# Kernel optimization log

Hardware: AMD Instinct MI355X
Metric: run time of the kernel (lower is better)

The kernel has to match this reference:

```python
import jax, jax.numpy as jnp
import numpy as np

KEY_SIZE = 256
EPS = 1e-8  # torch F.cosine_similarity default eps


def setup_inputs() -> dict:
    key = jax.random.key(0)
    k1, k2 = jax.random.split(key)
    B, M, K, V = 2048, 100000, KEY_SIZE, 256
    query = jax.random.normal(k1, (B, K), dtype=jnp.float32)
    memory = jax.random.normal(k2, (M, K + V), dtype=jnp.float32)
    return {"query": query, "memory": memory}


def reference(query, memory):
    # memory: [M, K+V] -> keys [M, K], values [M, V]
    keys = memory[:, :KEY_SIZE]
    values = memory[:, KEY_SIZE:]
    # cosine similarity: (q . k) / max(|q|*|k|, eps)  -> [B, M]
    dots = jnp.einsum('bk,mk->bm', query, keys)
    qn = jnp.linalg.norm(query, axis=1)  # [B]
    kn = jnp.linalg.norm(keys, axis=1)   # [M]
    sims = dots / jnp.maximum(qn[:, None] * kn[None, :], EPS)
    # top-1 over memory dim, then gather values -> [B, V]
    idx = jnp.argmax(sims, axis=1)
    return values[idx]
```

## Files before the change

kernel.cpp:

```cpp
#include <hip/hip_runtime.h>
#include <hip/hip_fp16.h>
#include <float.h>

#define MKEY 256
#define NMEM 100000
#define NPAD 100096
#define NQ   2048
#define BM 128
#define BN 128
#define NTILES 782
#define BLKPAD 800
#define MTILES 16
#define GRID (128 * 98)
#define KEYBLOCKS (NPAD / 4)
#define QS (127.0f / 6.0f)
#define SS2 ((6.0f / 127.0f) * (6.0f / 127.0f))

typedef int i32x4 __attribute__((ext_vector_type(4)));

__device__ inline void gll16(const void* g, void* l) {
  __builtin_amdgcn_global_load_lds(
      (const __attribute__((address_space(1))) unsigned*)g,
      (__attribute__((address_space(3))) unsigned*)l, 16, 0, 0);
}

__device__ inline int pack_i8x4(float4 v) {
  int c0 = max(-127, min(127, __float2int_rn(v.x * QS)));
  int c1 = max(-127, min(127, __float2int_rn(v.y * QS)));
  int c2 = max(-127, min(127, __float2int_rn(v.z * QS)));
  int c3 = max(-127, min(127, __float2int_rn(v.w * QS)));
  return (c0 & 255) | ((c1 & 255) << 8) | ((c2 & 255) << 16) | ((c3 & 255) << 24);
}

__device__ inline int dot4i8(int a, int b) {
  int s = 0;
#pragma unroll
  for (int k = 0; k < 4; ++k) {
    const int av = (a << (24 - 8 * k)) >> 24;
    const int bv = (b << (24 - 8 * k)) >> 24;
    s += av * bv;
  }
  return s;
}

__global__ void convert(const float* __restrict__ q, const float* __restrict__ mem,
                        int* __restrict__ qi, int* __restrict__ ki,
                        float* __restrict__ rkn) {
  const int b = blockIdx.x;
  if (b >= KEYBLOCKS) {
    const int i = (b - KEYBLOCKS) * 256 + threadIdx.x;
    const float4 v = *(const float4*)&q[(size_t)i * 4];
    qi[i] = pack_i8x4(v);
    return;
  }
  const int t = threadIdx.x, lane = t & 63, w = t >> 6;
  const int row = b * 4 + w;
  if (row < NMEM) {
    const float4 v = *(const float4*)&mem[(long)row * 512 + lane * 4];
    const float ss0 = v.x * v.x + v.y * v.y + v.z * v.z + v.w * v.w;
    ki[(size_t)row * 64 + lane] = pack_i8x4(v);
    float ss = ss0;
#pragma unroll
    for (int off = 32; off >= 1; off >>= 1) ss += __shfl_xor(ss, off, 64);
    if (lane == 0) rkn[row] = 1.0f / sqrtf(fmaxf(ss, 1e-30f));
  } else {
    ki[(size_t)row * 64 + lane] = 0;
    if (lane == 0) rkn[row] = 0.f;
  }
}

__global__ __launch_bounds__(256, 4) void gemm_screen(
    const int* __restrict__ qi, const int* __restrict__ ki,
    const float* __restrict__ rkn, float* __restrict__ bmaxB) {
  __shared__ __align__(128) char Ab[BM * 128];
  __shared__ __align__(128) char Bb[BN * 128];
  __shared__ float cand[BM][2];

  const int id = blockIdx.x;
  const int mtile = (id >> 3) & 15;
  const int ntile = (id & 7) + 8 * (id >> 7);
  if (ntile >= NTILES) return;

  const int t = threadIdx.x;
  const int w = t >> 6;
  const int lane = t & 63;
  const int wr = w >> 1, wc = w & 1;
  const int q16 = lane >> 4, l16 = lane & 15;
  const int l8 = lane >> 3, c8 = lane & 7;

  const int swz = (c8 ^ l8) * 16;
  int soff[8];
#pragma unroll
  for (int c = 0; c < 8; ++c)
    soff[c] = ((w & 1) * 64 + c * 8 + l8) * 256 + swz;
  const char* asrc = (const char*)((w < 2) ? qi : ki) +
                     (size_t)(((w < 2) ? mtile : ntile) * 128) * 256;
  char* adst = ((w < 2) ? Ab : Bb) + (w & 1) * 8192;

  i32x4 acc[4][4];
#pragma unroll
  for (int i = 0; i < 4; i++)
#pragma unroll
    for (int j = 0; j < 4; j++) acc[i][j] = (i32x4){0, 0, 0, 0};

  int pc[2];
#pragma unroll
  for (int ks = 0; ks < 2; ++ks) pc[ks] = (((ks * 4 + q16) ^ (l16 & 7))) * 16;

#pragma unroll
  for (int s = 0; s < 2; ++s) {
    __syncthreads();
#pragma unroll
    for (int c = 0; c < 8; ++c)
      gll16(asrc + s * 128 + soff[c], adst + c * 1024);
    __syncthreads();
#pragma unroll
    for (int ks = 0; ks < 2; ++ks) {
      i32x4 av[4], bv[4];
#pragma unroll
      for (int i = 0; i < 4; i++)
        av[i] = *(const i32x4*)&Ab[(64 * wr + 16 * i + l16) * 128 + pc[ks]];
#pragma unroll
      for (int j = 0; j < 4; j++)
        bv[j] = *(const i32x4*)&Bb[(64 * wc + 16 * j + l16) * 128 + pc[ks]];
#pragma unroll
      for (int i = 0; i < 4; i++)
#pragma unroll
        for (int j = 0; j < 4; j++)
          acc[i][j] = __builtin_amdgcn_mfma_i32_16x16x64_i8(av[i], bv[j], acc[i][j], 0, 0, 0);
    }
  }

  int ncol[4];
  float rk[4];
#pragma unroll
  for (int j = 0; j < 4; j++) {
    ncol[j] = ntile * BN + 64 * wc + 16 * j + l16;
    rk[j] = (ncol[j] < NMEM) ? rkn[ncol[j]] * SS2 : 0.f;
  }
#pragma unroll
  for (int i = 0; i < 4; i++) {
#pragma unroll
    for (int r = 0; r < 4; r++) {
      float m = -FLT_MAX;
#pragma unroll
      for (int j = 0; j < 4; j++)
        if (ncol[j] < NMEM) m = fmaxf(m, (float)acc[i][j][r] * rk[j]);
#pragma unroll
      for (int off = 1; off < 16; off <<= 1)
        m = fmaxf(m, __shfl_xor(m, off, 64));
      if (l16 == 0) cand[64 * wr + 16 * i + 4 * q16 + r][wc] = m;
    }
  }
  __syncthreads();
  if (t < BM) {
    float v = fmaxf(cand[t][0], cand[t][1]);
    bmaxB[(size_t)ntile * NQ + mtile * BM + t] = v;
  }
}

__global__ __launch_bounds__(256) void transpose_blk(const float* __restrict__ in,
                                                     float* __restrict__ outp) {
  __shared__ float tl[32][33];
  const int bid = blockIdx.x;
  const int ntt = bid % 25, qt = bid / 25;
  const int r0 = ntt * 32, c0 = qt * 32;
  const int tx = threadIdx.x & 31, ty = threadIdx.x >> 5;
#pragma unroll
  for (int k = 0; k < 4; ++k) {
    const int r = r0 + ty + 8 * k;
    tl[ty + 8 * k][tx] = (r < NTILES) ? in[(size_t)r * NQ + c0 + tx] : -FLT_MAX;
  }
  __syncthreads();
#pragma unroll
  for (int k = 0; k < 4; ++k) {
    const int qq = c0 + ty + 8 * k;
    const int nt = r0 + tx;
    if (nt < NTILES) outp[(size_t)qq * BLKPAD + nt] = tl[tx][ty + 8 * k];
  }
}

__global__ __launch_bounds__(256) void rescore_gather(
    const float* __restrict__ q, const float* __restrict__ mem,
    const int* __restrict__ qi8, const int* __restrict__ ki8,
    const float* __restrict__ rkn, const float* __restrict__ bmaxQ,
    float* __restrict__ out) {
  __shared__ float red2[4];
  __shared__ int blist[64];
  __shared__ int nblk;
  __shared__ int rlist[256];
  __shared__ int nrow;
  __shared__ double wb[4];
  __shared__ int wbi[4];
  __shared__ int widx;

  const int qid = blockIdx.x;
  const int t = threadIdx.x, w = t >> 6, lane = t & 63;

  const float4 qv = *(const float4*)&q[(size_t)qid * 256 + lane * 4];
  float ss = qv.x * qv.x + qv.y * qv.y + qv.z * qv.z + qv.w * qv.w;
#pragma unroll
  for (int off = 32; off >= 1; off >>= 1) ss += __shfl_xor(ss, off, 64);
  const float qn = sqrtf(ss);
  const float margin = 1.8e-2f * qn;

  int4 qreg[4];
#pragma unroll
  for (int k = 0; k < 4; ++k)
    qreg[k] = *(const int4*)&qi8[(size_t)qid * 64 + (lane & 3) * 16 + k * 4];

  if (t == 0) { nblk = 0; nrow = 0; }
  const float* bq = &bmaxQ[(size_t)qid * BLKPAD];

  float gm = -FLT_MAX;
  for (int i = t; i < NTILES; i += 256) gm = fmaxf(gm, bq[i]);
#pragma unroll
  for (int off = 32; off >= 1; off >>= 1) gm = fmaxf(gm, __shfl_xor(gm, off, 64));
  if (lane == 0) red2[w] = gm;
  __syncthreads();
  gm = fmaxf(fmaxf(red2[0], red2[1]), fmaxf(red2[2], red2[3]));
  const float thresh = gm - margin;

  for (int i = t; i < NTILES; i += 256)
    if (bq[i] >= thresh) {
      int p = atomicAdd(&nblk, 1);
      if (p < 64) blist[p] = i;
    }
  __syncthreads();
  const int nb_ = min(nblk, 64);

  for (int c = 0; c < nb_; ++c) {
    const int nt = blist[c];
#pragma unroll
    for (int pass = 0; pass < 2; ++pass) {
      const int row = nt * 128 + pass * 64 + w * 16 + (lane >> 2);
      int idot = 0;
      if (row < NMEM) {
#pragma unroll
        for (int k = 0; k < 4; ++k) {
          const int4 kv = *(const int4*)&ki8[(size_t)row * 64 + (lane & 3) * 16 + k * 4];
          idot += dot4i8(kv.x, qreg[k].x) + dot4i8(kv.y, qreg[k].y) +
                  dot4i8(kv.z, qreg[k].z) + dot4i8(kv.w, qreg[k].w);
        }
      }
      idot += __shfl_xor(idot, 1, 64);
      idot += __shfl_xor(idot, 2, 64);
      if ((lane & 3) == 0 && row < NMEM) {
        const float sh = (float)idot * (rkn[row] * SS2);
        if (sh >= thresh) {
          int p = atomicAdd(&nrow, 1);
          if (p < 256) rlist[p] = row;
        }
      }
    }
  }
  __syncthreads();
  const int nr = min(nrow, 256);

  double bestv = -1e300;
  int bestidx = 0x7fffffff;
  for (int c = w; c < nr; c += 4) {
    const int row = rlist[c];
    const float4 kv = *(const float4*)&mem[(size_t)row * 512 + lane * 4];
    double d = (double)kv.x * qv.x + (double)kv.y * qv.y +
               (double)kv.z * qv.z + (double)kv.w * qv.w;
    double s2 = (double)kv.x * kv.x + (double)kv.y * kv.y +
                (double)kv.z * kv.z + (double)kv.w * kv.w;
#pragma unroll
    for (int off = 32; off >= 1; off >>= 1) {
      d += __shfl_xor(d, off, 64);
      s2 += __shfl_xor(s2, off, 64);
    }
    if (lane == 0) {
      const double score = d / sqrt(s2 > 1e-300 ? s2 : 1e-300);
      if (score > bestv || (score == bestv && row < bestidx)) {
        bestv = score;
        bestidx = row;
      }
    }
  }
  if (lane == 0) { wb[w] = bestv; wbi[w] = bestidx; }
  __syncthreads();
  if (t == 0) {
    double bv = wb[0];
    int bi = wbi[0];
#pragma unroll
    for (int w2 = 1; w2 < 4; ++w2)
      if (wb[w2] > bv || (wb[w2] == bv && wbi[w2] < bi)) {
        bv = wb[w2];
        bi = wbi[w2];
      }
    widx = bi;
  }
  __syncthreads();
  out[(size_t)qid * 256 + t] = mem[(size_t)widx * 512 + 256 + t];
}

extern "C" void kernel_launch(void* const* d_in, const int* in_sizes, int n_in,
                              void* d_out, int out_size, void* d_ws, size_t ws_size,
                              hipStream_t stream) {
  const float* query = (const float*)d_in[0];
  const float* memory = (const float*)d_in[1];
  float* out = (float*)d_out;

  char* p = (char*)d_ws;
  int* qi = (int*)p; p += (size_t)NQ * 64 * 4;
  int* ki = (int*)p; p += (size_t)NPAD * 64 * 4;
  float* rkn = (float*)p; p += (size_t)NPAD * 4;
  float* bmaxB = (float*)p; p += (size_t)NTILES * NQ * 4;
  float* bmaxQ = (float*)p; p += (size_t)NQ * BLKPAD * 4;

  hipLaunchKernelGGL(convert, dim3(KEYBLOCKS + NQ * MKEY / 1024), dim3(256), 0, stream,
                     query, memory, qi, ki, rkn);
  hipLaunchKernelGGL(gemm_screen, dim3(GRID), dim3(256), 0, stream, qi, ki, rkn, bmaxB);
  hipLaunchKernelGGL(transpose_blk, dim3(25 * 64), dim3(256), 0, stream, bmaxB, bmaxQ);
  hipLaunchKernelGGL(rescore_gather, dim3(NQ), dim3(256), 0, stream,
                     query, memory, qi, ki, rkn, bmaxQ, out);
}
```

Measured before the change: 431.2 us.

## Add 16-row group maxima to screen rescoring and use sdot4 for int8 dots

The GEMM screen now also writes a per-(query, 16-key group) maximum of the int8 scores. It stages the accumulator tile through shared memory to compute both these maxima and the existing 128-key tile maxima. Rescoring first filters the candidate tiles down to 16-row groups that pass the threshold, so far fewer int8 key rows are re-dotted. The int8 dot product also uses the sdot4 builtin when it is available. The cost is an extra output array of roughly 51 MB written by the GEMM kernel and four more block barriers in its epilogue.

```diff
diff --git a/kernel.cpp b/kernel.cpp
--- a/kernel.cpp
+++ b/kernel.cpp
@@ -32,8 +32,10 @@
   return (c0 & 255) | ((c1 & 255) << 8) | ((c2 & 255) << 16) | ((c3 & 255) << 24);
 }
 
-__device__ inline int dot4i8(int a, int b) {
-  int s = 0;
+__device__ inline int dot4i8(int a, int b, int s) {
+#if __has_builtin(__builtin_amdgcn_sdot4)
+  return __builtin_amdgcn_sdot4(a, b, s, false);
+#else
 #pragma unroll
   for (int k = 0; k < 4; ++k) {
     const int av = (a << (24 - 8 * k)) >> 24;
@@ -41,6 +43,7 @@
     s += av * bv;
   }
   return s;
+#endif
 }
 
 __global__ void convert(const float* __restrict__ q, const float* __restrict__ mem,
@@ -71,10 +74,11 @@
 
 __global__ __launch_bounds__(256, 4) void gemm_screen(
     const int* __restrict__ qi, const int* __restrict__ ki,
-    const float* __restrict__ rkn, float* __restrict__ bmaxB) {
-  __shared__ __align__(128) char Ab[BM * 128];
-  __shared__ __align__(128) char Bb[BN * 128];
-  __shared__ float cand[BM][2];
+    const float* __restrict__ rkn,
+    float* __restrict__ bmax16B, float* __restrict__ bmaxB) {
+  __shared__ __align__(128) char smem[33792];
+  char* const Ab = smem;
+  char* const Bb = smem + 16384;
 
   const int id = blockIdx.x;
   const int mtile = (id >> 3) & 15;
@@ -131,31 +135,47 @@
     }
   }
 
-  int ncol[4];
   float rk[4];
 #pragma unroll
   for (int j = 0; j < 4; j++) {
-    ncol[j] = ntile * BN + 64 * wc + 16 * j + l16;
-    rk[j] = (ncol[j] < NMEM) ? rkn[ncol[j]] * SS2 : 0.f;
-  }
-#pragma unroll
-  for (int i = 0; i < 4; i++) {
-#pragma unroll
-    for (int r = 0; r < 4; r++) {
-      float m = -FLT_MAX;
-#pragma unroll
-      for (int j = 0; j < 4; j++)
-        if (ncol[j] < NMEM) m = fmaxf(m, (float)acc[i][j][r] * rk[j]);
-#pragma unroll
-      for (int off = 1; off < 16; off <<= 1)
-        m = fmaxf(m, __shfl_xor(m, off, 64));
-      if (l16 == 0) cand[64 * wr + 16 * i + 4 * q16 + r][wc] = m;
-    }
-  }
-  __syncthreads();
-  if (t < BM) {
-    float v = fmaxf(cand[t][0], cand[t][1]);
-    bmaxB[(size_t)ntile * NQ + mtile * BM + t] = v;
+    const int ncol = ntile * BN + 64 * wc + 16 * j + l16;
+    rk[j] = (ncol < NMEM) ? rkn[ncol] * SS2 : 0.f;
+  }
+  float (*L)[20] = (float(*)[20])smem;
+  float* bhalf = (float*)(smem + 32768);
+  const int wr_ = t >> 7, gg = (t >> 4) & 7, qrow = t & 15;
+  float outv[4];
+  __syncthreads();
+#pragma unroll
+  for (int i = 0; i < 4; ++i) {
+#pragma unroll
+    for (int j = 0; j < 4; ++j)
+#pragma unroll
+      for (int r = 0; r < 4; ++r)
+        L[(wr * 8 + wc * 4 + j) * 16 + q16 * 4 + r][l16] = (float)acc[i][j][r] * rk[j];
+    __syncthreads();
+    const float* Lr = L[(wr_ * 8 + gg) * 16 + qrow];
+    const float4 a = *(const float4*)&Lr[0], b4 = *(const float4*)&Lr[4];
+    const float4 cc = *(const float4*)&Lr[8], dd = *(const float4*)&Lr[12];
+    float m = fmaxf(fmaxf(fmaxf(a.x, a.y), fmaxf(a.z, a.w)),
+                    fmaxf(fmaxf(b4.x, b4.y), fmaxf(b4.z, b4.w)));
+    m = fmaxf(m, fmaxf(fmaxf(cc.x, cc.y), fmaxf(cc.z, cc.w)));
+    m = fmaxf(m, fmaxf(fmaxf(dd.x, dd.y), fmaxf(dd.z, dd.w)));
+    outv[i] = m;
+    float bm = fmaxf(m, __shfl_xor(m, 16, 64));
+    bm = fmaxf(bm, __shfl_xor(bm, 32, 64));
+    if (lane < 16) bhalf[(w * 16 + lane) * 4 + i] = bm;
+    __syncthreads();
+  }
+#pragma unroll
+  for (int i = 0; i < 4; ++i)
+    bmax16B[((size_t)ntile * NQ + mtile * 128 + wr_ * 64 + i * 16 + qrow) * 8 + gg] =
+        outv[i];
+  if (t < 128) {
+    const int wrb = t >> 6, ib = (t >> 4) & 3, qr = t & 15;
+    const float v = fmaxf(bhalf[((2 * wrb) * 16 + qr) * 4 + ib],
+                          bhalf[((2 * wrb + 1) * 16 + qr) * 4 + ib]);
+    bmaxB[(size_t)ntile * NQ + mtile * 128 + t] = v;
   }
 }
 
@@ -184,10 +204,12 @@
     const float* __restrict__ q, const float* __restrict__ mem,
     const int* __restrict__ qi8, const int* __restrict__ ki8,
     const float* __restrict__ rkn, const float* __restrict__ bmaxQ,
-    float* __restrict__ out) {
+    const float* __restrict__ bmax16B, float* __restrict__ out) {
   __shared__ float red2[4];
   __shared__ int blist[64];
   __shared__ int nblk;
+  __shared__ int glist[128];
+  __shared__ int ng;
   __shared__ int rlist[256];
   __shared__ int nrow;
   __shared__ double wb[4];
@@ -209,7 +231,7 @@
   for (int k = 0; k < 4; ++k)
     qreg[k] = *(const int4*)&qi8[(size_t)qid * 64 + (lane & 3) * 16 + k * 4];
 
-  if (t == 0) { nblk = 0; nrow = 0; }
+  if (t == 0) { nblk = 0; ng = 0; nrow = 0; }
   const float* bq = &bmaxQ[(size_t)qid * BLKPAD];
 
   float gm = -FLT_MAX;
@@ -229,28 +251,34 @@
   __syncthreads();
   const int nb_ = min(nblk, 64);
 
-  for (int c = 0; c < nb_; ++c) {
-    const int nt = blist[c];
-#pragma unroll
-    for (int pass = 0; pass < 2; ++pass) {
-      const int row = nt * 128 + pass * 64 + w * 16 + (lane >> 2);
-      int idot = 0;
-      if (row < NMEM) {
-#pragma unroll
-        for (int k = 0; k < 4; ++k) {
-          const int4 kv = *(const int4*)&ki8[(size_t)row * 64 + (lane & 3) * 16 + k * 4];
-          idot += dot4i8(kv.x, qreg[k].x) + dot4i8(kv.y, qreg[k].y) +
-                  dot4i8(kv.z, qreg[k].z) + dot4i8(kv.w, qreg[k].w);
-        }
-      }
-      idot += __shfl_xor(idot, 1, 64);
-      idot += __shfl_xor(idot, 2, 64);
-      if ((lane & 3) == 0 && row < NMEM) {
-        const float sh = (float)idot * (rkn[row] * SS2);
-        if (sh >= thresh) {
-          int p = atomicAdd(&nrow, 1);
-          if (p < 256) rlist[p] = row;
-        }
+  for (int idx = t; idx < nb_ * 8; idx += 256) {
+    const int nt = blist[idx >> 3], gl = idx & 7;
+    if (bmax16B[((size_t)nt * NQ + qid) * 8 + gl] >= thresh) {
+      int p = atomicAdd(&ng, 1);
+      if (p < 128) glist[p] = nt * 8 + gl;
+    }
+  }
+  __syncthreads();
+  const int ng_ = min(ng, 128);
+
+  for (int c = w; c < ng_; c += 4) {
+    const int row = glist[c] * 16 + (lane >> 2);
+    int idot = 0;
+#pragma unroll
+    for (int k = 0; k < 4; ++k) {
+      const int4 kv = *(const int4*)&ki8[(size_t)row * 64 + (lane & 3) * 16 + k * 4];
+      idot = dot4i8(kv.x, qreg[k].x, idot);
+      idot = dot4i8(kv.y, qreg[k].y, idot);
+      idot = dot4i8(kv.z, qreg[k].z, idot);
+      idot = dot4i8(kv.w, qreg[k].w, idot);
+    }
+    idot += __shfl_xor(idot, 1, 64);
+    idot += __shfl_xor(idot, 2, 64);
+    if ((lane & 3) == 0 && row < NMEM) {
+      const float sh = (float)idot * (rkn[row] * SS2);
+      if (sh >= thresh) {
+        int p = atomicAdd(&nrow, 1);
+        if (p < 256) rlist[p] = row;
       }
     }
   }
@@ -309,11 +337,13 @@
   float* rkn = (float*)p; p += (size_t)NPAD * 4;
   float* bmaxB = (float*)p; p += (size_t)NTILES * NQ * 4;
   float* bmaxQ = (float*)p; p += (size_t)NQ * BLKPAD * 4;
+  float* bmax16B = (float*)p; p += (size_t)NTILES * NQ * 32;
 
   hipLaunchKernelGGL(convert, dim3(KEYBLOCKS + NQ * MKEY / 1024), dim3(256), 0, stream,
                      query, memory, qi, ki, rkn);
-  hipLaunchKernelGGL(gemm_screen, dim3(GRID), dim3(256), 0, stream, qi, ki, rkn, bmaxB);
+  hipLaunchKernelGGL(gemm_screen, dim3(GRID), dim3(256), 0, stream,
+                     qi, ki, rkn, bmax16B, bmaxB);
   hipLaunchKernelGGL(transpose_blk, dim3(25 * 64), dim3(256), 0, stream, bmaxB, bmaxQ);
   hipLaunchKernelGGL(rescore_gather, dim3(NQ), dim3(256), 0, stream,
-                     query, memory, qi, ki, rkn, bmaxQ, out);
-}
+                     query, memory, qi, ki, rkn, bmaxQ, bmax16B, out);
+}
```

Result: faster. 369.0 us (-14.4%).
